# Kernel optimization log

Measured on AMD Instinct MI355X. Metric: run time of the kernel, lower is better.

The kernel has to match this reference:

```python
import jax, jax.numpy as jnp
import numpy as np
from jax.ops import segment_sum

N = 50000        # nodes
E = 800000       # edges
IN = 128         # in_channels
HID = 128        # hidden_channels
G = 256          # number of graphs


def setup_inputs() -> dict:
    key = jax.random.key(0)
    ks = jax.random.split(key, 24)

    def w(k, shape, fan_in):
        return (jax.random.normal(k, shape, dtype=jnp.float32) / np.sqrt(fan_in)).astype(jnp.float32)

    x = jax.random.normal(ks[0], (N, IN), dtype=jnp.float32)
    pos = jax.random.normal(ks[1], (N, 3), dtype=jnp.float32)
    edge_index = jax.random.randint(ks[2], (2, E), 0, N, dtype=jnp.int64)
    batch = jnp.sort(jax.random.randint(ks[3], (N,), 0, G, dtype=jnp.int64))

    params = dict(
        gcn_w=w(ks[4], (IN, HID), IN), gcn_b=jnp.zeros((HID,), jnp.float32),
        pam_w=w(ks[5], (IN, HID), IN), pam_b=jnp.zeros((HID,), jnp.float32),
        pm_w1=w(ks[6], (3, HID), 3), pm_b1=jnp.zeros((HID,), jnp.float32),
        pm_w2=w(ks[7], (HID, HID), HID), pm_b2=jnp.zeros((HID,), jnp.float32),
        att_w=w(ks[8], (2 * HID, 1), 2 * HID), att_b=jnp.zeros((1,), jnp.float32),
        fus_w=w(ks[9], (2 * HID, HID), 2 * HID), fus_b=jnp.zeros((HID,), jnp.float32),
        l1_w=w(ks[10], (HID, HID // 2), HID), l1_b=jnp.zeros((HID // 2,), jnp.float32),
        l2_w=w(ks[11], (HID // 2, 1), HID // 2), l2_b=jnp.zeros((1,), jnp.float32),
    )
    return dict(x=x, pos=pos, edge_index=edge_index, batch=batch, **params)


def reference(x, pos, edge_index, batch,
              gcn_w, gcn_b, pam_w, pam_b,
              pm_w1, pm_b1, pm_w2, pm_b2,
              att_w, att_b, fus_w, fus_b,
              l1_w, l1_b, l2_w, l2_b):
    n = x.shape[0]
    src, dst = edge_index[0], edge_index[1]  # j = source, i = target (PyG flow)

    # ---- global branch: GCNConv (self-loops + symmetric normalization) ----
    xw = x @ gcn_w                                   # [N, HID]
    loop = jnp.arange(n, dtype=src.dtype)
    s = jnp.concatenate([src, loop])
    d = jnp.concatenate([dst, loop])
    deg = segment_sum(jnp.ones_like(d, dtype=xw.dtype), d, num_segments=n)
    dinv = jnp.where(deg > 0, deg ** -0.5, 0.0)
    norm = dinv[s] * dinv[d]                          # [E+N]
    gcn = segment_sum(norm[:, None] * xw[s], d, num_segments=n) + gcn_b
    global_feat = jax.nn.relu(gcn)

    # ---- local branch: PAMConv ----
    xl = x @ pam_w + pam_b                            # [N, HID]
    x_i, x_j = xl[dst], xl[src]                       # [E, HID]
    delta = pos[dst] - pos[src]                       # [E, 3]
    de = jax.nn.relu(delta @ pm_w1 + pm_b1) @ pm_w2 + pm_b2   # [E, HID]
    att = jax.nn.sigmoid(jnp.concatenate([x_i, x_j], axis=-1) @ att_w + att_b)  # [E,1]
    msg = att * (x_j + de)
    local_feat = jax.nn.relu(segment_sum(msg, dst, num_segments=n))

    # ---- fusion + global mean pool + readout ----
    fused = jax.nn.relu(jnp.concatenate([global_feat, local_feat], axis=-1) @ fus_w + fus_b)
    counts = segment_sum(jnp.ones((n,), fused.dtype), batch, num_segments=G)
    pooled = segment_sum(fused, batch, num_segments=G) / jnp.clip(counts, 1.0)[:, None]
    h = jax.nn.relu(pooled @ l1_w + l1_b)
    return h @ l2_w + l2_b                            # [G, 1]
```

## Files before the change

kernel.cpp:

```cpp
#include <hip/hip_runtime.h>
#include <math.h>

#define NN 50000
#define NE 800000
#define HD 128
#define NG 256
#define SCAN_B 196
#define NODE_B 12500
#define HIST_B 3125
#define GEM_B 782
#define ZQ1 12512
#define ZQ2 8192

typedef unsigned int u32;
typedef unsigned short u16;
typedef __attribute__((ext_vector_type(8))) short bf16x8;
typedef __attribute__((ext_vector_type(4))) float f32x4;
typedef __attribute__((ext_vector_type(2))) float f32x2;

__device__ __forceinline__ float wave_allsum(float v) {
#pragma unroll
  for (int m = 1; m < 64; m <<= 1) v += __shfl_xor(v, m, 64);
  return v;
}
__device__ __forceinline__ float bcastf(float v, int t) {
  return __int_as_float(__builtin_amdgcn_readlane(__float_as_int(v), t));
}
__device__ __forceinline__ u32 f2b_bits(float f) {
  u32 u = __float_as_uint(f);
  return (u + 0x7fffu + ((u >> 16) & 1u)) >> 16;
}
__device__ __forceinline__ u32 pack2(float lo, float hi) {
  return f2b_bits(lo) | (f2b_bits(hi) << 16);
}
__device__ __forceinline__ f32x2 splat2(float v) { return (f32x2){v, v}; }
__device__ __forceinline__ f32x2 pkfma(f32x2 a, f32x2 b, f32x2 c) {
  return a * b + c;
}

__global__ __launch_bounds__(256) void k_wpack(
    const float* __restrict__ gcn_w, const float* __restrict__ pam_w,
    const float* __restrict__ pm_w2, const float* __restrict__ fus_w,
    const float* __restrict__ pam_b, const float* __restrict__ att_w,
    const float* __restrict__ att_b, const float* __restrict__ pm_b2,
    u16* __restrict__ Bg, u16* __restrict__ Bl, u16* __restrict__ Bf,
    float* __restrict__ vi, float* __restrict__ vj,
    float* __restrict__ consts, float* __restrict__ bsumv,
    uint4* __restrict__ zr1, uint4* __restrict__ zr2) {
  if (blockIdx.x >= 41) {
    int zi = (blockIdx.x - 41) * 256 + threadIdx.x;
    const uint4 z = {0u, 0u, 0u, 0u};
    if (zi < ZQ1) zr1[zi] = z;
    else if ((zi -= ZQ1) < ZQ2) zr2[zi] = z;
    return;
  }
  if (blockIdx.x == 40) {
    const int t = threadIdx.x;
    const int k = t & 127;
    const float* w = att_w + (t >> 7) * HD;
    float s = 0.f;
    for (int h = 0; h < HD; ++h) s = fmaf(pam_w[k * HD + h], w[h], s);
    if (t < 128) {
      vi[k] = s;
      bsumv[k] = pam_b[k] + pm_b2[k];
    } else {
      vj[k] = s;
    }
    if (t < 64) {
      float p = fmaf(pam_b[t], att_w[t], pam_b[t + 64] * att_w[t + 64]);
      p = wave_allsum(p);
      if (t == 0) consts[0] = p + att_b[0];
    } else if (t < 128) {
      const int l = t - 64;
      float p =
          fmaf(pam_b[l], att_w[HD + l], pam_b[l + 64] * att_w[HD + 64 + l]);
      p = wave_allsum(p);
      if (l == 0) consts[1] = p;
    }
    return;
  }
  const int t = blockIdx.x * 256 + threadIdx.x;
  const float* W;
  u16* dst;
  if (t < 2048) {
    const int kb = t >> 7, n = t & 127;
    W = gcn_w + (size_t)kb * 8 * HD + n;
    dst = Bg + (size_t)t * 8;
  } else if (t < 6144) {
    const int u = t - 2048;
    const int kb = u >> 7, n = u & 127;
    W = ((kb < 16) ? (pam_w + (size_t)kb * 8 * HD)
                   : (pm_w2 + (size_t)(kb - 16) * 8 * HD)) +
        n;
    dst = Bl + (size_t)u * 8;
  } else {
    const int u = t - 6144;
    const int kb = u >> 7, n = u & 127;
    W = fus_w + (size_t)kb * 8 * HD + n;
    dst = Bf + (size_t)u * 8;
  }
  union {
    u16 o[8];
    uint4 v;
  } pk;
#pragma unroll
  for (int i = 0; i < 8; ++i) pk.o[i] = (u16)f2b_bits(W[i * HD]);
  *(uint4*)dst = pk.v;
}

__global__ __launch_bounds__(256) void k_hist(const int* __restrict__ ei,
                                              int* __restrict__ cnt,
                                              u16* __restrict__ slot16) {
  int e = blockIdx.x * 256 + threadIdx.x;
  if (e < NE) slot16[e] = (u16)atomicAdd(&cnt[ei[NE + e]], 1);
}

__global__ __launch_bounds__(256) void k_scan1(const int* __restrict__ cnt,
                                               int* __restrict__ bsum) {
  const int i = blockIdx.x * 256 + threadIdx.x;
  int v = (i < NN) ? cnt[i] : 0;
#pragma unroll
  for (int m = 1; m < 64; m <<= 1) v += __shfl_xor(v, m, 64);
  __shared__ int s[4];
  if ((threadIdx.x & 63) == 0) s[threadIdx.x >> 6] = v;
  __syncthreads();
  if (threadIdx.x == 0) bsum[blockIdx.x] = s[0] + s[1] + s[2] + s[3];
}

__global__ __launch_bounds__(256) void k_scan23(
    const int* __restrict__ cnt, const int* __restrict__ bsum,
    const float* __restrict__ pos, int* __restrict__ offs,
    float* __restrict__ dinv, float4* __restrict__ pos4) {
  __shared__ int s[256];
  const int t = threadIdx.x;
  const int bv = (t < SCAN_B) ? bsum[t] : 0;
  s[t] = bv;
  __syncthreads();
  for (int d = 1; d < 256; d <<= 1) {
    int add = (t >= d) ? s[t - d] : 0;
    __syncthreads();
    s[t] += add;
    __syncthreads();
  }
  const int bpre = (blockIdx.x > 0) ? s[blockIdx.x - 1] : 0;
  __syncthreads();
  const int i = blockIdx.x * 256 + t;
  const int v = (i < NN) ? cnt[i] : 0;
  s[t] = v;
  __syncthreads();
  for (int d = 1; d < 256; d <<= 1) {
    int add = (t >= d) ? s[t - d] : 0;
    __syncthreads();
    s[t] += add;
    __syncthreads();
  }
  if (i < NN) {
    offs[i] = bpre + s[t] - v;
    dinv[i] = __builtin_amdgcn_rsqf((float)v + 1.0f);
    pos4[i] = make_float4(pos[3 * i], pos[3 * i + 1], pos[3 * i + 2], 0.f);
  }
}

__global__ __launch_bounds__(256) void k_scatgc(
    const int* __restrict__ ei, const int* __restrict__ offs,
    const u16* __restrict__ slot16, int* __restrict__ csr_src,
    const int* __restrict__ batch, float* __restrict__ counts,
    const float* __restrict__ x, const float* __restrict__ dinv,
    const int* __restrict__ cnt, const float* __restrict__ vi,
    const float* __restrict__ vj, const float* __restrict__ consts,
    u16* __restrict__ xq, float* __restrict__ ai_arr,
    float2* __restrict__ adj2) {
  if (blockIdx.x < HIST_B) {
    const int e = blockIdx.x * 256 + threadIdx.x;
    if (e < NE) {
      const int d = ei[NE + e];
      __builtin_nontemporal_store(ei[e], &csr_src[offs[d] + slot16[e]]);
    }
    return;
  }
  if (blockIdx.x == HIST_B) {
    const int g = threadIdx.x;
    int lo = 0, hi = NN;
    while (lo < hi) {
      const int mid = (lo + hi) >> 1;
      if (batch[mid] < g) lo = mid + 1; else hi = mid;
    }
    const int b0 = lo;
    hi = NN;
    while (lo < hi) {
      const int mid = (lo + hi) >> 1;
      if (batch[mid] <= g) lo = mid + 1; else hi = mid;
    }
    counts[g] = (float)(lo - b0);
    return;
  }
  const int wave = threadIdx.x >> 6, lane = threadIdx.x & 63;
  const int i = (blockIdx.x - HIST_B - 1) * 4 + wave;
  if (i >= NN) return;
  const float2 v = *(const float2*)&x[(size_t)i * HD + lane * 2];
  const float dv = dinv[i];
  const u32 q = __builtin_amdgcn_cvt_pk_fp8_f32(dv * v.x, dv * v.y, 0u, false);
  xq[(size_t)i * 64 + lane] = (u16)q;
  const float2 a = *(const float2*)&vi[lane * 2];
  const float2 b = *(const float2*)&vj[lane * 2];
  float si = wave_allsum(fmaf(v.x, a.x, v.y * a.y));
  float sj = wave_allsum(fmaf(v.x, b.x, v.y * b.y));
  if (lane == 0) {
    ai_arr[i] = si + consts[0];
    adj2[i] = make_float2(sj + consts[1], sqrtf((float)cnt[i] + 1.0f));
  }
}

__global__ __launch_bounds__(256) void k_agg(
    const u16* __restrict__ xq, const float4* __restrict__ pos4,
    const float2* __restrict__ adj2, const int* __restrict__ csr_src,
    const int* __restrict__ offs, const int* __restrict__ cnt,
    const float* __restrict__ ai_arr, const float* __restrict__ pm_w1,
    const float* __restrict__ pm_b1, u32* __restrict__ ZG,
    u32* __restrict__ XT, float* __restrict__ sa_out) {
  const int wave = threadIdx.x >> 6, lane = threadIdx.x & 63;
  const int i = blockIdx.x * 4 + wave;
  if (i >= NN) return;
  const int c0 = lane * 2;

  const f32x2 w1x = *(const f32x2*)&pm_w1[c0];
  const f32x2 w1y = *(const f32x2*)&pm_w1[HD + c0];
  const f32x2 w1z = *(const f32x2*)&pm_w1[2 * HD + c0];
  const f32x2 b1 = *(const f32x2*)&pm_b1[c0];
  const float ai = ai_arr[i];
  const float4 pi = pos4[i];
  const u16* xql = xq + lane;

  f32x2 zg = {0.f, 0.f}, xa = {0.f, 0.f}, tt = {0.f, 0.f};
  float sa = 0.f;
  const int b = offs[i], e = b + cnt[i];
  for (int base = b; base < e; base += 64) {
    const int mm = min(64, e - base);
    const int sk = csr_src[base + ((lane < mm) ? lane : 0)];
    const float2 a2 = adj2[sk];
    float attk = __builtin_amdgcn_rcpf(1.f + __expf(-(ai + a2.x)));
    const float4 ps = pos4[sk];
    const float apk = attk * a2.y;
    const float dxk = pi.x - ps.x;
    const float dyk = pi.y - ps.y;
    const float dzk = pi.z - ps.z;
    if (lane >= mm) attk = 0.f;
    sa += wave_allsum(attk);

    for (int s16 = 0; s16 < mm; s16 += 16) {
      const int n16 = min(16, mm - s16);
      u32 rr[16];
#pragma unroll
      for (int u = 0; u < 16; ++u) {
        if (u < n16) {
          const int s = __builtin_amdgcn_readlane(sk, s16 + u);
          rr[u] = xql[(size_t)s << 6];
        }
      }
#pragma unroll
      for (int u = 0; u < 16; ++u) {
        if (u < n16) {
          const int T = s16 + u;
          const float att = bcastf(attk, T);
          const float ap = bcastf(apk, T);
          const float dx = bcastf(dxk, T);
          const float dy = bcastf(dyk, T);
          const float dz = bcastf(dzk, T);
          const f32x2 y = __builtin_amdgcn_cvt_pk_f32_fp8(rr[u], false);
          zg += y;
          xa = pkfma(splat2(ap), y, xa);
          f32x2 gg = pkfma(splat2(dz), w1z,
                           pkfma(splat2(dy), w1y,
                                 pkfma(splat2(dx), w1x, b1)));
          gg = __builtin_elementwise_max(gg, splat2(0.f));
          tt = pkfma(splat2(att), gg, tt);
        }
      }
    }
  }
  const u32 xi = xql[(size_t)i << 6];
  zg += __builtin_amdgcn_cvt_pk_f32_fp8(xi, false);

  ZG[(size_t)i * 64 + lane] = pack2(zg.x, zg.y);
  XT[(size_t)i * 128 + lane] = pack2(xa.x, xa.y);
  XT[(size_t)i * 128 + 64 + lane] = pack2(tt.x, tt.y);
  if (lane == 0) sa_out[i] = sa;
}

template <int K16>
__device__ __forceinline__ void phase_g(const u16* __restrict__ pa,
                                        const u16* __restrict__ pb0,
                                        f32x4 acc[8]) {
  bf16x8 a[2], b[2][8];
  a[0] = *(const bf16x8*)pa;
#pragma unroll
  for (int cf = 0; cf < 8; ++cf) b[0][cf] = *(const bf16x8*)(pb0 + cf * 128);
#pragma unroll
  for (int k0 = 0; k0 < K16; ++k0) {
    if (k0 + 1 < K16) {
      a[(k0 + 1) & 1] = *(const bf16x8*)(pa + (k0 + 1) * 32);
      const u16* pn = pb0 + (size_t)(k0 + 1) * 4096;
#pragma unroll
      for (int cf = 0; cf < 8; ++cf)
        b[(k0 + 1) & 1][cf] = *(const bf16x8*)(pn + cf * 128);
    }
#pragma unroll
    for (int cf = 0; cf < 8; ++cf)
      acc[cf] = __builtin_amdgcn_mfma_f32_16x16x32_bf16(
          a[k0 & 1], b[k0 & 1][cf], acc[cf], 0, 0, 0);
  }
}

__global__ __launch_bounds__(256, 3) void k_gemms(
    const u16* __restrict__ ZG, const u16* __restrict__ XT,
    const u16* __restrict__ Bg, const u16* __restrict__ Bl,
    const u16* __restrict__ Bf, const float* __restrict__ dinv,
    const float* __restrict__ sa, const float* __restrict__ gcn_b,
    const float* __restrict__ bsumv, const float* __restrict__ fus_b,
    const int* __restrict__ batch, float* __restrict__ pooled) {
  __shared__ u16 T[64 * 256];
  __shared__ int batch_lds[64];
  const int n0 = blockIdx.x * 64;
  const int t = threadIdx.x, lane = t & 63, w = t >> 6;
  const int m = lane & 15, g = lane >> 4;
  const int r0 = w * 16;

  if (t < 64) batch_lds[t] = (n0 + t < NN) ? batch[n0 + t] : -1;

  float dv[4], sv[4];
#pragma unroll
  for (int j = 0; j < 4; ++j) {
    const int rr = min(n0 + r0 + g * 4 + j, NN - 1);
    dv[j] = dinv[rr];
    sv[j] = sa[rr];
  }
  float bgv[8], bsv[8];
#pragma unroll
  for (int cf = 0; cf < 8; ++cf) {
    bgv[cf] = gcn_b[cf * 16 + m];
    bsv[cf] = bsumv[cf * 16 + m];
  }

  const int rowA = min(n0 + r0 + m, NN - 1);
  f32x4 acc[8];

#pragma unroll
  for (int cf = 0; cf < 8; ++cf) acc[cf] = (f32x4){0.f, 0.f, 0.f, 0.f};
  phase_g<4>(ZG + (size_t)rowA * 128 + g * 8, Bg + ((size_t)g * HD + m) * 8,
             acc);
#pragma unroll
  for (int j = 0; j < 4; ++j) {
    const int rl = r0 + g * 4 + j;
#pragma unroll
    for (int cf = 0; cf < 8; ++cf) {
      const float v = fmaxf(fmaf(dv[j], acc[cf][j], bgv[cf]), 0.f);
      T[rl * 256 + ((cf * 16 + m) ^ ((rl & 7) << 3))] = (u16)f2b_bits(v);
    }
  }

#pragma unroll
  for (int cf = 0; cf < 8; ++cf) acc[cf] = (f32x4){0.f, 0.f, 0.f, 0.f};
  phase_g<8>(XT + (size_t)rowA * 256 + g * 8, Bl + ((size_t)g * HD + m) * 8,
             acc);
#pragma unroll
  for (int j = 0; j < 4; ++j) {
    const int rl = r0 + g * 4 + j;
#pragma unroll
    for (int cf = 0; cf < 8; ++cf) {
      const float v = fmaxf(fmaf(sv[j], bsv[cf], acc[cf][j]), 0.f);
      T[rl * 256 + ((128 + cf * 16 + m) ^ ((rl & 7) << 3))] = (u16)f2b_bits(v);
    }
  }

  const int x0m = (m & 7) << 3;
  const u16* rowT = &T[(r0 + m) * 256];
  const u16* pbC = Bf + ((size_t)g * HD + m) * 8;
#pragma unroll
  for (int cf = 0; cf < 8; ++cf) acc[cf] = (f32x4){0.f, 0.f, 0.f, 0.f};
  {
    bf16x8 a[2], b[2][8];
    a[0] = *(const bf16x8*)&rowT[(g * 8) ^ x0m];
#pragma unroll
    for (int cf = 0; cf < 8; ++cf) b[0][cf] = *(const bf16x8*)(pbC + cf * 128);
#pragma unroll
    for (int k0 = 0; k0 < 8; ++k0) {
      if (k0 + 1 < 8) {
        a[(k0 + 1) & 1] = *(const bf16x8*)&rowT[(g * 8 + (k0 + 1) * 32) ^ x0m];
        const u16* pn = pbC + (size_t)(k0 + 1) * 4096;
#pragma unroll
        for (int cf = 0; cf < 8; ++cf)
          b[(k0 + 1) & 1][cf] = *(const bf16x8*)(pn + cf * 128);
      }
#pragma unroll
      for (int cf = 0; cf < 8; ++cf)
        acc[cf] = __builtin_amdgcn_mfma_f32_16x16x32_bf16(
            a[k0 & 1], b[k0 & 1][cf], acc[cf], 0, 0, 0);
    }
  }
  float* F = (float*)T;
#pragma unroll
  for (int j = 0; j < 4; ++j) {
    const int rl = r0 + g * 4 + j;
#pragma unroll
    for (int cf = 0; cf < 8; ++cf)
      F[rl * 128 + ((cf * 16 + m) ^ ((rl & 12) << 2))] =
          fmaxf(acc[cf][j] + fus_b[cf * 16 + m], 0.f);
  }
  __syncthreads();

  const int col = t & 127;
  const int q = t >> 7;
  int seg = -1;
  float run = 0.f;
  for (int r = q * 32; r < q * 32 + 32; ++r) {
    const int bg = batch_lds[r];
    const float v = F[r * 128 + (col ^ ((r & 12) << 2))];
    if (bg != seg) {
      if (seg >= 0) atomicAdd(&pooled[seg * HD + col], run);
      seg = bg;
      run = 0.f;
    }
    if (bg >= 0) run += v;
  }
  if (seg >= 0) atomicAdd(&pooled[seg * HD + col], run);
}

__global__ __launch_bounds__(64) void k_head(const float* __restrict__ pooled,
                                             const float* __restrict__ counts,
                                             const float* __restrict__ l1w,
                                             const float* __restrict__ l1b,
                                             const float* __restrict__ l2w,
                                             const float* __restrict__ l2b,
                                             float* __restrict__ out) {
  const int g = blockIdx.x, j = threadIdx.x;
  const float inv = __builtin_amdgcn_rcpf(fmaxf(counts[g], 1.f));
  float acc = l1b[j];
  for (int k = 0; k < HD; ++k)
    acc = fmaf(pooled[g * HD + k] * inv, l1w[k * 64 + j], acc);
  float v = fmaxf(acc, 0.f) * l2w[j];
  v = wave_allsum(v);
  if (j == 0) out[g] = v + l2b[0];
}

extern "C" void kernel_launch(void* const* d_in, const int* in_sizes, int n_in,
                              void* d_out, int out_size, void* d_ws,
                              size_t ws_size, hipStream_t stream) {
  const float* x = (const float*)d_in[0];
  const float* pos = (const float*)d_in[1];
  const int* ei = (const int*)d_in[2];
  const int* batch = (const int*)d_in[3];
  const float* gcn_w = (const float*)d_in[4];
  const float* gcn_b = (const float*)d_in[5];
  const float* pam_w = (const float*)d_in[6];
  const float* pam_b = (const float*)d_in[7];
  const float* pm_w1 = (const float*)d_in[8];
  const float* pm_b1 = (const float*)d_in[9];
  const float* pm_w2 = (const float*)d_in[10];
  const float* pm_b2 = (const float*)d_in[11];
  const float* att_w = (const float*)d_in[12];
  const float* att_b = (const float*)d_in[13];
  const float* fus_w = (const float*)d_in[14];
  const float* fus_b = (const float*)d_in[15];
  const float* l1_w = (const float*)d_in[16];
  const float* l1_b = (const float*)d_in[17];
  const float* l2_w = (const float*)d_in[18];
  const float* l2_b = (const float*)d_in[19];
  float* out = (float*)d_out;

  size_t off = 0;
  auto alloc = [&](size_t bytes) {
    void* p = (char*)d_ws + off;
    off += (bytes + 255) & ~size_t(255);
    return p;
  };
  u16* xq = (u16*)alloc((size_t)NN * 64 * 2);
  u32* ZG = (u32*)alloc((size_t)NN * 64 * 4);
  u32* XT = (u32*)alloc((size_t)NN * 128 * 4);
  float* sa = (float*)alloc((size_t)NN * 4);
  float* ai = (float*)alloc((size_t)NN * 4);
  float* dinv = (float*)alloc((size_t)NN * 4);
  float2* adj2 = (float2*)alloc((size_t)NN * 8);
  float4* pos4 = (float4*)alloc((size_t)NN * 16);
  float* pooled = (float*)alloc((size_t)NG * HD * 4);
  float* counts = (float*)alloc((size_t)NG * 4);
  int* cnt = (int*)alloc((size_t)NN * 4);
  int* offs = (int*)alloc((size_t)NN * 4);
  int* csr_src = (int*)alloc((size_t)NE * 4);
  u16* slot16 = (u16*)alloc((size_t)NE * 2);
  int* bsum = (int*)alloc((size_t)SCAN_B * 4);
  u16* Bg = (u16*)alloc((size_t)16 * 128 * 8 * 2);
  u16* Bl = (u16*)alloc((size_t)32 * 128 * 8 * 2);
  u16* Bf = (u16*)alloc((size_t)32 * 128 * 8 * 2);
  float* vi = (float*)alloc(128 * 4);
  float* vj = (float*)alloc(128 * 4);
  float* consts = (float*)alloc(2 * 4);
  float* bsumv = (float*)alloc(128 * 4);

  k_wpack<<<41 + (ZQ1 + ZQ2 + 255) / 256, 256, 0, stream>>>(
      gcn_w, pam_w, pm_w2, fus_w, pam_b, att_w, att_b, pm_b2, Bg, Bl, Bf, vi,
      vj, consts, bsumv, (uint4*)cnt, (uint4*)pooled);
  k_hist<<<HIST_B, 256, 0, stream>>>(ei, cnt, slot16);
  k_scan1<<<SCAN_B, 256, 0, stream>>>(cnt, bsum);
  k_scan23<<<SCAN_B, 256, 0, stream>>>(cnt, bsum, pos, offs, dinv, pos4);
  k_scatgc<<<HIST_B + 1 + NODE_B, 256, 0, stream>>>(
      ei, offs, slot16, csr_src, batch, counts, x, dinv, cnt, vi, vj, consts,
      xq, ai, adj2);
  k_agg<<<NODE_B, 256, 0, stream>>>(xq, pos4, adj2, csr_src, offs, cnt, ai,
                                    pm_w1, pm_b1, ZG, XT, sa);
  k_gemms<<<GEM_B, 256, 0, stream>>>((const u16*)ZG, (const u16*)XT, Bg, Bl,
                                     Bf, dinv, sa, gcn_b, bsumv, fus_b, batch,
                                     pooled);
  k_head<<<NG, 64, 0, stream>>>(pooled, counts, l1_w, l1_b, l2_w, l2_b, out);
}
```

Baseline: 174.0 us.

## Split node aggregation across two waves, fuse histogram into weight-pack kernel

The aggregation kernel now gives each node two waves. Each wave handles half of the node's incoming edges, and the partial sums are combined through shared memory. This raises memory-level parallelism for the gather-bound loop, at the cost of a block-wide barrier and extra LDS traffic. Separately, the edge histogram moves into the weight-pack launch, the cnt zeroing moves to hipMemsetAsync, a hardware packed bf16 convert replaces the manual rounding, and the nontemporal store on the CSR scatter is dropped. There is a correctness risk: the histogram blocks in the same launch assume cnt is zeroed beforehand, which the memset now handles.

```diff
diff --git a/kernel.cpp b/kernel.cpp
--- a/kernel.cpp
+++ b/kernel.cpp
@@ -7,10 +7,11 @@
 #define NG 256
 #define SCAN_B 196
 #define NODE_B 12500
+#define AGG_B 25000
 #define HIST_B 3125
 #define GEM_B 782
-#define ZQ1 12512
 #define ZQ2 8192
+#define WP_HIST0 73
 
 typedef unsigned int u32;
 typedef unsigned short u16;
@@ -30,8 +31,10 @@
   u32 u = __float_as_uint(f);
   return (u + 0x7fffu + ((u >> 16) & 1u)) >> 16;
 }
-__device__ __forceinline__ u32 pack2(float lo, float hi) {
-  return f2b_bits(lo) | (f2b_bits(hi) << 16);
+__device__ __forceinline__ u32 cvtpk_bf16(float lo, float hi) {
+  u32 r;
+  asm("v_cvt_pk_bf16_f32 %0, %1, %2" : "=v"(r) : "v"(lo), "v"(hi));
+  return r;
 }
 __device__ __forceinline__ f32x2 splat2(float v) { return (f32x2){v, v}; }
 __device__ __forceinline__ f32x2 pkfma(f32x2 a, f32x2 b, f32x2 c) {
@@ -46,12 +49,16 @@
     u16* __restrict__ Bg, u16* __restrict__ Bl, u16* __restrict__ Bf,
     float* __restrict__ vi, float* __restrict__ vj,
     float* __restrict__ consts, float* __restrict__ bsumv,
-    uint4* __restrict__ zr1, uint4* __restrict__ zr2) {
+    uint4* __restrict__ zr2, const int* __restrict__ ei,
+    int* __restrict__ cnt, u16* __restrict__ slot16) {
+  if (blockIdx.x >= WP_HIST0) {
+    const int e = (blockIdx.x - WP_HIST0) * 256 + threadIdx.x;
+    if (e < NE) slot16[e] = (u16)atomicAdd(&cnt[ei[NE + e]], 1);
+    return;
+  }
   if (blockIdx.x >= 41) {
-    int zi = (blockIdx.x - 41) * 256 + threadIdx.x;
-    const uint4 z = {0u, 0u, 0u, 0u};
-    if (zi < ZQ1) zr1[zi] = z;
-    else if ((zi -= ZQ1) < ZQ2) zr2[zi] = z;
+    const int zi = (blockIdx.x - 41) * 256 + threadIdx.x;
+    if (zi < ZQ2) zr2[zi] = (uint4){0u, 0u, 0u, 0u};
     return;
   }
   if (blockIdx.x == 40) {
@@ -108,13 +115,6 @@
   *(uint4*)dst = pk.v;
 }
 
-__global__ __launch_bounds__(256) void k_hist(const int* __restrict__ ei,
-                                              int* __restrict__ cnt,
-                                              u16* __restrict__ slot16) {
-  int e = blockIdx.x * 256 + threadIdx.x;
-  if (e < NE) slot16[e] = (u16)atomicAdd(&cnt[ei[NE + e]], 1);
-}
-
 __global__ __launch_bounds__(256) void k_scan1(const int* __restrict__ cnt,
                                                int* __restrict__ bsum) {
   const int i = blockIdx.x * 256 + threadIdx.x;
@@ -174,7 +174,7 @@
     const int e = blockIdx.x * 256 + threadIdx.x;
     if (e < NE) {
       const int d = ei[NE + e];
-      __builtin_nontemporal_store(ei[e], &csr_src[offs[d] + slot16[e]]);
+      csr_src[offs[d] + slot16[e]] = ei[e];
     }
     return;
   }
@@ -218,9 +218,10 @@
     const float* __restrict__ ai_arr, const float* __restrict__ pm_w1,
     const float* __restrict__ pm_b1, u32* __restrict__ ZG,
     u32* __restrict__ XT, float* __restrict__ sa_out) {
-  const int wave = threadIdx.x >> 6, lane = threadIdx.x & 63;
-  const int i = blockIdx.x * 4 + wave;
-  if (i >= NN) return;
+  __shared__ float part[2][64][9];
+  const int w = threadIdx.x >> 6, lane = threadIdx.x & 63;
+  const int nl = w >> 1, half = w & 1;
+  const int i = blockIdx.x * 2 + nl;
   const int c0 = lane * 2;
 
   const f32x2 w1x = *(const f32x2*)&pm_w1[c0];
@@ -229,13 +230,15 @@
   const f32x2 b1 = *(const f32x2*)&pm_b1[c0];
   const float ai = ai_arr[i];
   const float4 pi = pos4[i];
-  const u16* xql = xq + lane;
 
   f32x2 zg = {0.f, 0.f}, xa = {0.f, 0.f}, tt = {0.f, 0.f};
   float sa = 0.f;
-  const int b = offs[i], e = b + cnt[i];
-  for (int base = b; base < e; base += 64) {
-    const int mm = min(64, e - base);
+  const int b = offs[i], c = cnt[i];
+  const int hf = (c + 1) >> 1;
+  const int lo = b + (half ? hf : 0);
+  const int hiE = half ? (b + c) : (b + hf);
+  for (int base = lo; base < hiE; base += 64) {
+    const int mm = min(64, hiE - base);
     const int sk = csr_src[base + ((lane < mm) ? lane : 0)];
     const float2 a2 = adj2[sk];
     float attk = __builtin_amdgcn_rcpf(1.f + __expf(-(ai + a2.x)));
@@ -254,7 +257,7 @@
       for (int u = 0; u < 16; ++u) {
         if (u < n16) {
           const int s = __builtin_amdgcn_readlane(sk, s16 + u);
-          rr[u] = xql[(size_t)s << 6];
+          rr[u] = *(xq + ((size_t)s << 6) + lane);
         }
       }
 #pragma unroll
@@ -278,13 +281,27 @@
       }
     }
   }
-  const u32 xi = xql[(size_t)i << 6];
-  zg += __builtin_amdgcn_cvt_pk_f32_fp8(xi, false);
-
-  ZG[(size_t)i * 64 + lane] = pack2(zg.x, zg.y);
-  XT[(size_t)i * 128 + lane] = pack2(xa.x, xa.y);
-  XT[(size_t)i * 128 + 64 + lane] = pack2(tt.x, tt.y);
-  if (lane == 0) sa_out[i] = sa;
+  if (half) {
+    float* p = part[nl][lane];
+    p[0] = zg.x; p[1] = zg.y;
+    p[2] = xa.x; p[3] = xa.y;
+    p[4] = tt.x; p[5] = tt.y;
+    p[6] = sa;
+  }
+  __syncthreads();
+  if (!half) {
+    const float* p = part[nl][lane];
+    zg.x += p[0]; zg.y += p[1];
+    xa.x += p[2]; xa.y += p[3];
+    tt.x += p[4]; tt.y += p[5];
+    sa += p[6];
+    const u32 xi = *(xq + ((size_t)i << 6) + lane);
+    zg += __builtin_amdgcn_cvt_pk_f32_fp8(xi, false);
+    ZG[(size_t)i * 64 + lane] = cvtpk_bf16(zg.x, zg.y);
+    XT[(size_t)i * 128 + lane] = cvtpk_bf16(xa.x, xa.y);
+    XT[(size_t)i * 128 + 64 + lane] = cvtpk_bf16(tt.x, tt.y);
+    if (lane == 0) sa_out[i] = sa;
+  }
 }
 
 template <int K16>
@@ -496,17 +513,17 @@
   float* consts = (float*)alloc(2 * 4);
   float* bsumv = (float*)alloc(128 * 4);
 
-  k_wpack<<<41 + (ZQ1 + ZQ2 + 255) / 256, 256, 0, stream>>>(
+  hipMemsetAsync(cnt, 0, NN * 4, stream);
+  k_wpack<<<WP_HIST0 + HIST_B, 256, 0, stream>>>(
       gcn_w, pam_w, pm_w2, fus_w, pam_b, att_w, att_b, pm_b2, Bg, Bl, Bf, vi,
-      vj, consts, bsumv, (uint4*)cnt, (uint4*)pooled);
-  k_hist<<<HIST_B, 256, 0, stream>>>(ei, cnt, slot16);
+      vj, consts, bsumv, (uint4*)pooled, ei, cnt, slot16);
   k_scan1<<<SCAN_B, 256, 0, stream>>>(cnt, bsum);
   k_scan23<<<SCAN_B, 256, 0, stream>>>(cnt, bsum, pos, offs, dinv, pos4);
   k_scatgc<<<HIST_B + 1 + NODE_B, 256, 0, stream>>>(
       ei, offs, slot16, csr_src, batch, counts, x, dinv, cnt, vi, vj, consts,
       xq, ai, adj2);
-  k_agg<<<NODE_B, 256, 0, stream>>>(xq, pos4, adj2, csr_src, offs, cnt, ai,
-                                    pm_w1, pm_b1, ZG, XT, sa);
+  k_agg<<<AGG_B, 256, 0, stream>>>(xq, pos4, adj2, csr_src, offs, cnt, ai,
+                                   pm_w1, pm_b1, ZG, XT, sa);
   k_gemms<<<GEM_B, 256, 0, stream>>>((const u16*)ZG, (const u16*)XT, Bg, Bl,
                                      Bf, dinv, sa, gcn_b, bsumv, fus_b, batch,
                                      pooled);
```

Measured after the change: 170.1 us. 1.02x faster.
